# Optimization experiments

Hardware: AMD Instinct MI355X
Metric: run time of the kernel (lower is better)

## Reference

```python
import math
import jax, jax.numpy as jnp
import numpy as np

NUM_HEADS = 16
TAU_RCS, LAMBDA_RCS = 2.0, 0.6
PATCH = 16
PREFIX = 8
GAUSS_STD = 5.0


def gaussian_window(d1, d2, std):
    c = 1.0 / (std * math.sqrt(2.0))
    k1 = (jnp.arange(d1, dtype=jnp.float32) - (d1 - 1) / 2.0) * c
    k2 = (jnp.arange(d2, dtype=jnp.float32) - (d2 - 1) / 2.0) * c
    return jnp.exp(-(k1[:, None] ** 2 + k2[None, :] ** 2))  # [d1, d2]


def attention_addition(d1, d2, prefix, std):
    # out[(a,b),(c,d)] = window[a-c+d1-1, b-d+d2-1]  (conv of delta images with window)
    win = gaussian_window(2 * d1 - 1, 2 * d2 - 1, std)
    ia = jnp.arange(d1)
    jb = jnp.arange(d2)
    r = ia[:, None] - ia[None, :] + (d1 - 1)   # [d1, d1]
    s = jb[:, None] - jb[None, :] + (d2 - 1)   # [d2, d2]
    add = win[r[:, None, :, None], s[None, :, None, :]]  # [d1,d2,d1,d2]
    add = add.reshape(d1 * d2, d1 * d2)
    add = jnp.pad(add, ((prefix, 0), (prefix, 0)))  # zero rows/cols for prefix tokens
    return add[None]  # [1, N, N]


def setup_inputs() -> dict:
    key = jax.random.key(0)
    ks = jax.random.split(key, 5)
    B, C = 4, 1024
    d1 = d2 = 512 // PATCH  # 32
    N = d1 * d2 + PREFIX    # 1032
    H = NUM_HEADS
    x = jax.random.normal(ks[0], (B, N, C), dtype=jnp.float32)
    qkv_w = jax.random.normal(ks[1], (3 * C, C), dtype=jnp.float32) * 0.02
    qkv_b = jnp.zeros((3 * C,), dtype=jnp.float32)
    proj_w = jax.random.normal(ks[2], (C, C), dtype=jnp.float32) * 0.02
    proj_b = jnp.zeros((C,), dtype=jnp.float32)
    attn_add = attention_addition(d1, d2, PREFIX, GAUSS_STD)
    # stored RCS attention maps are softmax outputs -> row-normalized positives
    rcs = jax.random.uniform(ks[3], (B * H, N, N), dtype=jnp.float32)
    rcs = rcs / jnp.sum(rcs, axis=-1, keepdims=True)
    return {"x": x, "qkv_w": qkv_w, "qkv_b": qkv_b, "proj_w": proj_w,
            "proj_b": proj_b, "attn_addition": attn_add, "rcs_attn": rcs}


def reference(x, qkv_w, qkv_b, proj_w, proj_b, attn_addition, rcs_attn):
    B, N, C = x.shape
    H = NUM_HEADS
    hd = C // H
    scale = hd ** -0.5
    qkv = jnp.einsum('bnc,dc->bnd', x, qkv_w) + qkv_b  # [B,N,3C]
    q, k, v = jnp.split(qkv, 3, axis=-1)
    def to_heads(t):
        return t.reshape(B, N, H, hd).transpose(0, 2, 1, 3).reshape(B * H, N, hd)
    k = to_heads(k)
    v = to_heads(v)
    # custom K-K attention with additive Gaussian bias
    attn = jnp.einsum('bnd,bmd->bnm', k, k) * scale + attn_addition
    attn = jax.nn.softmax(attn, axis=-1)
    # RCS blending with stored intermediate attention maps
    attn = TAU_RCS * ((1.0 - LAMBDA_RCS) * attn + LAMBDA_RCS * rcs_attn)
    out = jnp.einsum('bnm,bmd->bnd', attn, v)  # [B*H, N, hd]
    out = out.reshape(B, H, N, hd).transpose(0, 2, 1, 3).reshape(B, N, C)
    out = jnp.einsum('bnc,dc->bnd', out, proj_w) + proj_b
    return out
```

## Files before the change

kernel.cpp:

```cpp
#include <hip/hip_runtime.h>
#include <stdint.h>

#define NSEQ 1032
#define CDIM 1024
#define HD 64
#define H_HEADS 16
#define BROWS 4128
#define SCALE 0.125f

typedef __attribute__((ext_vector_type(8))) short bf16x8;
typedef __attribute__((ext_vector_type(4))) float f32x4;

__device__ __forceinline__ unsigned short f2bf(float f) {
  union { float f; uint32_t u; } c; c.f = f;
  uint32_t u = c.u;
  return (unsigned short)((u + 0x7fffu + ((u >> 16) & 1u)) >> 16);
}

__device__ __forceinline__ void gl16(const void* gp, void* lp) {
  __builtin_amdgcn_global_load_lds((const __attribute__((address_space(1))) void*)gp,
                                   (__attribute__((address_space(3))) void*)lp, 16, 0, 0);
}

__global__ void convert_f32_bf16(const float* __restrict__ src, unsigned short* __restrict__ dst, int n4) {
  int i = blockIdx.x * blockDim.x + threadIdx.x;
  if (i >= n4) return;
  float4 v = ((const float4*)src)[i];
  ushort4 o;
  o.x = f2bf(v.x); o.y = f2bf(v.y); o.z = f2bf(v.z); o.w = f2bf(v.w);
  ((ushort4*)dst)[i] = o;
}

template<int MODE>
__global__ __launch_bounds__(256, 2) void gemm_bt(
    const unsigned short* __restrict__ A,
    const unsigned short* __restrict__ Bw,
    const float* __restrict__ bias,
    unsigned short* __restrict__ outK,
    unsigned short* __restrict__ outV,
    float* __restrict__ outF,
    int M, int K)
{
  __shared__ unsigned short As[128 * 32];
  __shared__ unsigned short Bs[128 * 32];
  const int t = threadIdx.x;
  const int w = t >> 6, lane = t & 63, lr = lane & 15, lg = lane >> 4;
  const int wr = w >> 1, wc = w & 1;
  const int m0 = blockIdx.y * 128, n0 = blockIdx.x * 128;
  f32x4 acc[4][4] = {};

  for (int ks = 0; ks < K; ks += 32) {
    #pragma unroll
    for (int q = 0; q < 2; ++q) {
      const int o = t + (q << 8);
      const int row = o >> 2, kc = o & 3;
      int ra = m0 + row; ra = ra < M ? ra : M - 1;
      gl16(A + (size_t)ra * K + ks + kc * 8, (void*)(As + o * 8));
      gl16(Bw + (size_t)(n0 + row) * K + ks + kc * 8, (void*)(Bs + o * 8));
    }
    __syncthreads();
    bf16x8 af[4], bfr[4];
    #pragma unroll
    for (int m = 0; m < 4; ++m)
      af[m] = *(const bf16x8*)(As + (wr * 64 + m * 16 + lr) * 32 + lg * 8);
    #pragma unroll
    for (int n = 0; n < 4; ++n)
      bfr[n] = *(const bf16x8*)(Bs + (wc * 64 + n * 16 + lr) * 32 + lg * 8);
    #pragma unroll
    for (int m = 0; m < 4; ++m)
      #pragma unroll
      for (int n = 0; n < 4; ++n)
        acc[m][n] = __builtin_amdgcn_mfma_f32_16x16x32_bf16(af[m], bfr[n], acc[m][n], 0, 0, 0);
    __syncthreads();
  }

  #pragma unroll
  for (int m = 0; m < 4; ++m) {
    const int rowb = m0 + wr * 64 + m * 16 + lg * 4;
    #pragma unroll
    for (int n = 0; n < 4; ++n) {
      const int col = n0 + wc * 64 + n * 16 + lr;
      const float bv = bias[col];
      #pragma unroll
      for (int r = 0; r < 4; ++r) {
        const int row = rowb + r;
        if (row >= M) continue;
        const float v = acc[m][n][r] + bv;
        if (MODE == 0) {
          const int b = row / NSEQ, nn = row - b * NSEQ;
          if (col < CDIM) {
            const int h = col >> 6, d = col & 63;
            outK[((size_t)(b * H_HEADS + h) * NSEQ + nn) * HD + d] = f2bf(v);
          } else {
            const int jj = col - CDIM, h = jj >> 6, d = jj & 63;
            outV[((size_t)(b * H_HEADS + h) * HD + d) * NSEQ + nn] = f2bf(v);
          }
        } else {
          outF[(size_t)row * CDIM + col] = v;
        }
      }
    }
  }
}

__global__ __launch_bounds__(256, 2) void attn_fused(
    const unsigned short* __restrict__ Kb,
    const unsigned short* __restrict__ Vt,
    const float* __restrict__ rcs,
    unsigned short* __restrict__ outp)
{
  __shared__ __align__(16) unsigned short Kc[2][64 * 64];
  __shared__ __align__(16) unsigned short Vs[2][64 * 64];
  __shared__ __align__(16) float As[2][64 * 64];
  __shared__ unsigned short Ps[64 * 72];
  const int t = threadIdx.x;
  const int w = t >> 6, lane = t & 63, lr = lane & 15, lg = lane >> 4;
  const int bid = blockIdx.x;
  const int nb = (bid & 7) * 136 + (bid >> 3);
  const int bh = nb / 17, rt = nb - bh * 17;
  const int i_base = rt * 64 + w * 16;
  const int arow = w * 16 + lr;
  const float* rbase = rcs + (size_t)bh * NSEQ * NSEQ;
  const unsigned short* kbase = Kb + (size_t)bh * NSEQ * HD;
  const unsigned short* vbase = Vt + (size_t)bh * HD * NSEQ;

  const unsigned short* srck[2]; int dok[2];
  const unsigned short* srcv[2]; int dov[2];
  const float* srca[4]; int doa[4];
  #pragma unroll
  for (int q = 0; q < 2; ++q) {
    const int p = t + (q << 8);
    const int row = p >> 3, sch = p & 7;
    const int gch = (sch ^ row) & 7;
    srck[q] = kbase + (size_t)row * HD + gch * 8;  dok[q] = p * 8;
    srcv[q] = vbase + (size_t)row * NSEQ + gch * 8; dov[q] = p * 8;
  }
  #pragma unroll
  for (int q = 0; q < 4; ++q) {
    const int p = t + (q << 8);
    const int row = p >> 4, sch = p & 15;
    const int gch = (sch & 8) | ((sch ^ row) & 7);
    int grow = rt * 64 + row; if (grow > NSEQ - 1) grow = NSEQ - 1;
    srca[q] = rbase + (size_t)grow * NSEQ + gch * 4;  doa[q] = p * 4;
  }

  auto stage_fast = [&](int tB, int buf) {
    #pragma unroll
    for (int q = 0; q < 2; ++q) gl16(srck[q] + (size_t)tB * HD, (void*)(Kc[buf] + dok[q]));
    #pragma unroll
    for (int q = 0; q < 2; ++q) gl16(srcv[q] + tB, (void*)(Vs[buf] + dov[q]));
    #pragma unroll
    for (int q = 0; q < 4; ++q) gl16(srca[q] + tB, (void*)(As[buf] + doa[q]));
  };
  auto stage_tail = [&](int buf) {
    const int tB = 1024;
    #pragma unroll
    for (int q = 0; q < 2; ++q) {
      const int p = t + (q << 8);
      const int row = p >> 3, sch = p & 7;
      const int gch = (sch ^ row) & 7;
      int mrow = tB + row; if (mrow > NSEQ - 1) mrow = NSEQ - 1;
      gl16(kbase + (size_t)mrow * HD + gch * 8, (void*)(Kc[buf] + p * 8));
    }
    #pragma unroll
    for (int q = 0; q < 2; ++q) {
      const int p = t + (q << 8);
      const int row = p >> 3, sch = p & 7;
      const int gch = (sch ^ row) & 7;
      int gc = tB + gch * 8; if (gc > NSEQ - 8) gc = NSEQ - 8;
      gl16(vbase + (size_t)row * NSEQ + gc, (void*)(Vs[buf] + p * 8));
    }
    #pragma unroll
    for (int q = 0; q < 4; ++q) {
      const int p = t + (q << 8);
      const int row = p >> 4, sch = p & 15;
      const int gch = (sch & 8) | ((sch ^ row) & 7);
      int grow = rt * 64 + row; if (grow > NSEQ - 1) grow = NSEQ - 1;
      int gcol = tB + gch * 4; if (gcol > NSEQ - 4) gcol = NSEQ - 4;
      gl16(rbase + (size_t)grow * NSEQ + gcol, (void*)(As[buf] + p * 4));
    }
  };

  bf16x8 akr[2];
  {
    int row = i_base + lr; if (row > NSEQ - 1) row = NSEQ - 1;
    const unsigned short* p = kbase + (size_t)row * HD + lg * 8;
    akr[0] = *(const bf16x8*)(p);
    akr[1] = *(const bf16x8*)(p + 32);
  }

  const int irow_base = i_base + lg * 4;
  float u[16], v[16];
  {
    #pragma unroll
    for (int fn = 0; fn < 4; ++fn) {
      const int x = 16 * fn + lr;
      const int m1_0 = ((x + 24) >> 5) - 1;
      const int m2 = (x - 8) & 31;
      #pragma unroll
      for (int r = 0; r < 4; ++r) {
        const int irow = irow_base + r;
        const int ip = irow - 8;
        const int i1 = ip >> 5, j1 = ip & 31;
        const int di = i1 - m1_0, dj = j1 - m2;
        const float iok = (irow >= 8) ? 1.f : 0.f;
        u[fn * 4 + r] = __expf(-0.02f * (float)(di * di + dj * dj)) * iok;
        v[fn * 4 + r] = __expf(0.08f * (float)di);
      }
    }
  }
  const float C1 = 0.92311634639f;
  const float C2 = 0.85214378896f;

  f32x4 accP[4] = {};
  f32x4 accR[4] = {};
  float lsum[4] = {0.f, 0.f, 0.f, 0.f};

  stage_fast(0, 0);
  asm volatile("s_waitcnt vmcnt(0)");
  __builtin_amdgcn_s_barrier();
  __builtin_amdgcn_sched_barrier(0);

  for (int mt = 0; mt < 17; ++mt) {
    const int mB = mt * 64;
    const int cur = mt & 1, nxt = cur ^ 1;

    if (mt < 15)      stage_fast(mB + 64, nxt);
    else if (mt == 15) stage_tail(nxt);

    const unsigned short* kc = Kc[cur];
    const unsigned short* vsb = Vs[cur];

    __builtin_amdgcn_s_setprio(1);
    f32x4 s[4];
    #pragma unroll
    for (int fn = 0; fn < 4; ++fn) {
      const int row = 16 * fn + lr;
      const int r7 = row & 7;
      f32x4 z = {0.f, 0.f, 0.f, 0.f};
      bf16x8 b0 = *(const bf16x8*)(kc + row * 64 + ((lg ^ r7) & 7) * 8);
      bf16x8 b1 = *(const bf16x8*)(kc + row * 64 + (((4 + lg) ^ r7) & 7) * 8);
      z = __builtin_amdgcn_mfma_f32_16x16x32_bf16(akr[0], b0, z, 0, 0, 0);
      z = __builtin_amdgcn_mfma_f32_16x16x32_bf16(akr[1], b1, z, 0, 0, 0);
      s[fn] = z;
    }
    __builtin_amdgcn_s_setprio(0);

    #pragma unroll
    for (int fn = 0; fn < 4; ++fn) {
      const int mcol = mB + 16 * fn + lr;
      const float mok = (mcol >= 8 && mcol < NSEQ) ? 1.f : 0.f;
      const bool mlt = (mcol < NSEQ);
      #pragma unroll
      for (int r = 0; r < 4; ++r) {
        const int fi = fn * 4 + r;
        const float sv = s[fn][r] * SCALE + u[fi] * mok;
        const float p = mlt ? __expf(sv) : 0.f;
        lsum[r] += p;
        Ps[(w * 16 + lg * 4 + r) * 72 + 16 * fn + lr] = f2bf(p);
        u[fi] *= v[fi] * C1;
        v[fi] *= C2;
      }
    }

    bf16x8 af[2];
    #pragma unroll
    for (int kf = 0; kf < 2; ++kf) {
      bf16x8 a;
      const int kg = mB + kf * 32 + lg * 8;
      if (kg + 8 <= NSEQ) {
        const float* ab = As[cur] + arow * 64;
        const int c0 = kf * 8 + 2 * lg;
        const int s0 = (c0 & 8) | ((c0 ^ arow) & 7);
        const int s1 = (c0 & 8) | (((c0 + 1) ^ arow) & 7);
        f32x4 lo = *(const f32x4*)(ab + s0 * 4);
        f32x4 hi = *(const f32x4*)(ab + s1 * 4);
        a[0] = (short)f2bf(lo[0]); a[1] = (short)f2bf(lo[1]);
        a[2] = (short)f2bf(lo[2]); a[3] = (short)f2bf(lo[3]);
        a[4] = (short)f2bf(hi[0]); a[5] = (short)f2bf(hi[1]);
        a[6] = (short)f2bf(hi[2]); a[7] = (short)f2bf(hi[3]);
      } else {
        #pragma unroll
        for (int j = 0; j < 8; ++j) a[j] = 0;
      }
      af[kf] = a;
    }

    bf16x8 pa0 = *(const bf16x8*)(Ps + (w * 16 + lr) * 72 + lg * 8);
    bf16x8 pa1 = *(const bf16x8*)(Ps + (w * 16 + lr) * 72 + 32 + lg * 8);
    __builtin_amdgcn_s_setprio(1);
    #pragma unroll
    for (int fd = 0; fd < 4; ++fd) {
      const int row = 16 * fd + lr;
      const int r7 = row & 7;
      bf16x8 v0 = *(const bf16x8*)(vsb + row * 64 + ((lg ^ r7) & 7) * 8);
      bf16x8 v1 = *(const bf16x8*)(vsb + row * 64 + (((4 + lg) ^ r7) & 7) * 8);
      accP[fd] = __builtin_amdgcn_mfma_f32_16x16x32_bf16(pa0, v0, accP[fd], 0, 0, 0);
      accP[fd] = __builtin_amdgcn_mfma_f32_16x16x32_bf16(pa1, v1, accP[fd], 0, 0, 0);
      accR[fd] = __builtin_amdgcn_mfma_f32_16x16x32_bf16(af[0], v0, accR[fd], 0, 0, 0);
      accR[fd] = __builtin_amdgcn_mfma_f32_16x16x32_bf16(af[1], v1, accR[fd], 0, 0, 0);
    }
    __builtin_amdgcn_s_setprio(0);

    __builtin_amdgcn_sched_barrier(0);
    asm volatile("s_waitcnt vmcnt(0)");
    __builtin_amdgcn_s_barrier();
    __builtin_amdgcn_sched_barrier(0);
  }

  #pragma unroll
  for (int r = 0; r < 4; ++r) {
    float vv = lsum[r];
    vv += __shfl_xor(vv, 1); vv += __shfl_xor(vv, 2);
    vv += __shfl_xor(vv, 4); vv += __shfl_xor(vv, 8);
    lsum[r] = vv;
  }

  const int b = bh >> 4, hh = bh & 15;
  #pragma unroll
  for (int fd = 0; fd < 4; ++fd) {
    #pragma unroll
    for (int r = 0; r < 4; ++r) {
      const int irow = i_base + lg * 4 + r;
      if (irow < NSEQ) {
        const float val = 0.8f * accP[fd][r] / lsum[r] + 1.2f * accR[fd][r];
        outp[(size_t)(b * NSEQ + irow) * CDIM + hh * 64 + 16 * fd + lr] = f2bf(val);
      }
    }
  }
}

extern "C" void kernel_launch(void* const* d_in, const int* in_sizes, int n_in,
                              void* d_out, int out_size, void* d_ws, size_t ws_size,
                              hipStream_t stream) {
  (void)in_sizes; (void)n_in; (void)out_size; (void)ws_size;
  const float* x      = (const float*)d_in[0];
  const float* qkv_w  = (const float*)d_in[1];
  const float* qkv_b  = (const float*)d_in[2];
  const float* proj_w = (const float*)d_in[3];
  const float* proj_b = (const float*)d_in[4];
  const float* rcs    = (const float*)d_in[6];
  float* out = (float*)d_out;

  char* ws = (char*)d_ws;
  unsigned short* x_bf = (unsigned short*)ws; ws += (size_t)BROWS * CDIM * 2;
  unsigned short* wkv  = (unsigned short*)ws; ws += (size_t)2048 * CDIM * 2;
  unsigned short* wp   = (unsigned short*)ws; ws += (size_t)1024 * CDIM * 2;
  unsigned short* Kb   = (unsigned short*)ws; ws += (size_t)64 * NSEQ * HD * 2;
  unsigned short* Vt   = (unsigned short*)ws; ws += (size_t)64 * HD * NSEQ * 2;
  unsigned short* op   = (unsigned short*)ws; ws += (size_t)BROWS * CDIM * 2;

  const int n1 = BROWS * CDIM / 4, n2 = 2048 * CDIM / 4, n3 = 1024 * CDIM / 4;
  convert_f32_bf16<<<(n1 + 255) / 256, 256, 0, stream>>>(x, x_bf, n1);
  convert_f32_bf16<<<(n2 + 255) / 256, 256, 0, stream>>>(qkv_w + 1024 * 1024, wkv, n2);
  convert_f32_bf16<<<(n3 + 255) / 256, 256, 0, stream>>>(proj_w, wp, n3);

  gemm_bt<0><<<dim3(16, 33), 256, 0, stream>>>(x_bf, wkv, qkv_b + 1024, Kb, Vt, nullptr, BROWS, CDIM);
  attn_fused<<<1088, 256, 0, stream>>>(Kb, Vt, rcs, op);
  gemm_bt<1><<<dim3(8, 33), 256, 0, stream>>>(op, wp, proj_b, nullptr, nullptr, out, BROWS, CDIM);
}
```

Baseline: 197.4 us.

## Prefetch RCS tile through registers into a single bf16 LDS buffer; raise occupancy

The fp32 double-buffered RCS tile staged by direct global-to-LDS loads is replaced. Each thread now prefetches the next RCS slice into registers and converts it to bf16. It writes the result into a single padded bf16 LDS buffer after the MFMA phase. This cuts LDS use from roughly 73KB to 50KB per block, and launch bounds are raised to 3 blocks per CU to hide the memory-bound RCS stream. The cost is more live registers under a tighter register budget, so spills are possible.

Measured after the change: 178.1 us. -9.8%, faster.

```diff
diff --git a/kernel.cpp b/kernel.cpp
--- a/kernel.cpp
+++ b/kernel.cpp
@@ -103,7 +103,7 @@
   }
 }
 
-__global__ __launch_bounds__(256, 2) void attn_fused(
+__global__ __launch_bounds__(256, 3) void attn_fused(
     const unsigned short* __restrict__ Kb,
     const unsigned short* __restrict__ Vt,
     const float* __restrict__ rcs,
@@ -111,7 +111,7 @@
 {
   __shared__ __align__(16) unsigned short Kc[2][64 * 64];
   __shared__ __align__(16) unsigned short Vs[2][64 * 64];
-  __shared__ __align__(16) float As[2][64 * 64];
+  __shared__ __align__(16) unsigned short As[64 * 72];
   __shared__ unsigned short Ps[64 * 72];
   const int t = threadIdx.x;
   const int w = t >> 6, lane = t & 63, lr = lane & 15, lg = lane >> 4;
@@ -126,7 +126,6 @@
 
   const unsigned short* srck[2]; int dok[2];
   const unsigned short* srcv[2]; int dov[2];
-  const float* srca[4]; int doa[4];
   #pragma unroll
   for (int q = 0; q < 2; ++q) {
     const int p = t + (q << 8);
@@ -135,24 +134,13 @@
     srck[q] = kbase + (size_t)row * HD + gch * 8;  dok[q] = p * 8;
     srcv[q] = vbase + (size_t)row * NSEQ + gch * 8; dov[q] = p * 8;
   }
-  #pragma unroll
-  for (int q = 0; q < 4; ++q) {
-    const int p = t + (q << 8);
-    const int row = p >> 4, sch = p & 15;
-    const int gch = (sch & 8) | ((sch ^ row) & 7);
-    int grow = rt * 64 + row; if (grow > NSEQ - 1) grow = NSEQ - 1;
-    srca[q] = rbase + (size_t)grow * NSEQ + gch * 4;  doa[q] = p * 4;
-  }
-
-  auto stage_fast = [&](int tB, int buf) {
+  auto stage_kv = [&](int tB, int buf) {
     #pragma unroll
     for (int q = 0; q < 2; ++q) gl16(srck[q] + (size_t)tB * HD, (void*)(Kc[buf] + dok[q]));
     #pragma unroll
     for (int q = 0; q < 2; ++q) gl16(srcv[q] + tB, (void*)(Vs[buf] + dov[q]));
-    #pragma unroll
-    for (int q = 0; q < 4; ++q) gl16(srca[q] + tB, (void*)(As[buf] + doa[q]));
   };
-  auto stage_tail = [&](int buf) {
+  auto stage_kv_tail = [&](int buf) {
     const int tB = 1024;
     #pragma unroll
     for (int q = 0; q < 2; ++q) {
@@ -170,14 +158,29 @@
       int gc = tB + gch * 8; if (gc > NSEQ - 8) gc = NSEQ - 8;
       gl16(vbase + (size_t)row * NSEQ + gc, (void*)(Vs[buf] + p * 8));
     }
-    #pragma unroll
-    for (int q = 0; q < 4; ++q) {
-      const int p = t + (q << 8);
-      const int row = p >> 4, sch = p & 15;
-      const int gch = (sch & 8) | ((sch ^ row) & 7);
-      int grow = rt * 64 + row; if (grow > NSEQ - 1) grow = NSEQ - 1;
-      int gcol = tB + gch * 4; if (gcol > NSEQ - 4) gcol = NSEQ - 4;
-      gl16(rbase + (size_t)grow * NSEQ + gcol, (void*)(As[buf] + p * 4));
+  };
+
+  const int ccol = (lane & 15) * 4;
+  const float* rsrc[4]; int lrow_loc[4];
+  #pragma unroll
+  for (int j = 0; j < 4; ++j) {
+    lrow_loc[j] = w * 16 + j * 4 + (lane >> 4);
+    int grow = rt * 64 + lrow_loc[j]; if (grow > NSEQ - 1) grow = NSEQ - 1;
+    rsrc[j] = rbase + (size_t)grow * NSEQ;
+  }
+  f32x4 rreg[4];
+  auto ld_rcs = [&](int tB) {
+    int gcol = tB + ccol; if (gcol > NSEQ - 4) gcol = NSEQ - 4;
+    #pragma unroll
+    for (int j = 0; j < 4; ++j) rreg[j] = *(const f32x4*)(rsrc[j] + gcol);
+  };
+  auto wr_rcs = [&]() {
+    #pragma unroll
+    for (int j = 0; j < 4; ++j) {
+      ushort4 o;
+      o.x = f2bf(rreg[j][0]); o.y = f2bf(rreg[j][1]);
+      o.z = f2bf(rreg[j][2]); o.w = f2bf(rreg[j][3]);
+      *(ushort4*)(As + lrow_loc[j] * 72 + ccol) = o;
     }
   };
 
@@ -216,7 +219,9 @@
   f32x4 accR[4] = {};
   float lsum[4] = {0.f, 0.f, 0.f, 0.f};
 
-  stage_fast(0, 0);
+  ld_rcs(0);
+  stage_kv(0, 0);
+  wr_rcs();
   asm volatile("s_waitcnt vmcnt(0)");
   __builtin_amdgcn_s_barrier();
   __builtin_amdgcn_sched_barrier(0);
@@ -225,8 +230,9 @@
     const int mB = mt * 64;
     const int cur = mt & 1, nxt = cur ^ 1;
 
-    if (mt < 15)      stage_fast(mB + 64, nxt);
-    else if (mt == 15) stage_tail(nxt);
+    if (mt < 16)       ld_rcs(mB + 64);
+    if (mt < 15)       stage_kv(mB + 64, nxt);
+    else if (mt == 15) stage_kv_tail(nxt);
 
     const unsigned short* kc = Kc[cur];
     const unsigned short* vsb = Vs[cur];
@@ -266,24 +272,13 @@
     bf16x8 af[2];
     #pragma unroll
     for (int kf = 0; kf < 2; ++kf) {
-      bf16x8 a;
       const int kg = mB + kf * 32 + lg * 8;
       if (kg + 8 <= NSEQ) {
-        const float* ab = As[cur] + arow * 64;
-        const int c0 = kf * 8 + 2 * lg;
-        const int s0 = (c0 & 8) | ((c0 ^ arow) & 7);
-        const int s1 = (c0 & 8) | (((c0 + 1) ^ arow) & 7);
-        f32x4 lo = *(const f32x4*)(ab + s0 * 4);
-        f32x4 hi = *(const f32x4*)(ab + s1 * 4);
-        a[0] = (short)f2bf(lo[0]); a[1] = (short)f2bf(lo[1]);
-        a[2] = (short)f2bf(lo[2]); a[3] = (short)f2bf(lo[3]);
-        a[4] = (short)f2bf(hi[0]); a[5] = (short)f2bf(hi[1]);
-        a[6] = (short)f2bf(hi[2]); a[7] = (short)f2bf(hi[3]);
+        af[kf] = *(const bf16x8*)(As + arow * 72 + kf * 32 + lg * 8);
       } else {
         #pragma unroll
-        for (int j = 0; j < 8; ++j) a[j] = 0;
-      }
-      af[kf] = a;
+        for (int j = 0; j < 8; ++j) af[kf][j] = 0;
+      }
     }
 
     bf16x8 pa0 = *(const bf16x8*)(Ps + (w * 16 + lr) * 72 + lg * 8);
@@ -301,6 +296,8 @@
       accR[fd] = __builtin_amdgcn_mfma_f32_16x16x32_bf16(af[1], v1, accR[fd], 0, 0, 0);
     }
     __builtin_amdgcn_s_setprio(0);
+
+    if (mt < 16) wr_rcs();
 
     __builtin_amdgcn_sched_barrier(0);
     asm volatile("s_waitcnt vmcnt(0)");
```
